# Kernel tuning notes

Hardware: AMD Instinct MI355X
Metric: run time of the kernel (lower is better)

The kernel has to match this reference:

```python
import jax, jax.numpy as jnp
import numpy as np

N = 50000   # nodes
E = 800000  # edges (avg degree 16)
D = 128     # embedding_size
K = 4096    # number of candidate result nodes (resmask.sum())


def setup_inputs() -> dict:
    key = jax.random.key(0)
    ks = jax.random.split(key, 14)
    scale = 1.0 / np.sqrt(D)
    input_node = jax.random.normal(ks[0], (N, D), jnp.float32)
    inputad = jax.random.randint(ks[1], (2, E), 0, N, dtype=jnp.int32)
    res = jax.random.uniform(ks[2], (N,), jnp.float32)
    # first-K-ones mask so masked_select has a static shape [K, D]
    resmask = jnp.concatenate([jnp.ones((K,), jnp.int32), jnp.zeros((N - K,), jnp.int32)])
    params = dict(
        W1=jax.random.normal(ks[3], (D, D), jnp.float32) * scale,
        a_src1=jax.random.normal(ks[4], (D,), jnp.float32) * scale,
        a_dst1=jax.random.normal(ks[5], (D,), jnp.float32) * scale,
        b1=jnp.zeros((D,), jnp.float32),
        W2=jax.random.normal(ks[6], (D, D), jnp.float32) * scale,
        a_src2=jax.random.normal(ks[7], (D,), jnp.float32) * scale,
        a_dst2=jax.random.normal(ks[8], (D,), jnp.float32) * scale,
        b2=jnp.zeros((D,), jnp.float32),
        w_lin=jax.random.normal(ks[9], (D,), jnp.float32) * scale,
        b_lin=jnp.zeros((), jnp.float32),
    )
    return dict(input_node=input_node, inputad=inputad, res=res,
                resmask=resmask, num_res=K, **params)


def _gat_layer(x, src, dst, W, a_src, a_dst, b):
    """PyG GATConv, heads=1, concat=False, negative_slope=0.2."""
    n = x.shape[0]
    h = x @ W                          # [N, D]
    alpha_src = h @ a_src              # [N]
    alpha_dst = h @ a_dst              # [N]
    e = jax.nn.leaky_relu(alpha_src[src] + alpha_dst[dst], 0.2)  # [E']
    # softmax over incoming edges per destination node (stable)
    emax = jax.ops.segment_max(e, dst, num_segments=n)
    ee = jnp.exp(e - emax[dst])
    denom = jax.ops.segment_sum(ee, dst, num_segments=n)
    alpha = ee / (denom[dst] + 1e-16)
    out = jax.ops.segment_sum(h[src] * alpha[:, None], dst, num_segments=n)
    return out + b


def reference(input_node, inputad, res, resmask, num_res,
              W1, a_src1, a_dst1, b1, W2, a_src2, a_dst2, b2, w_lin, b_lin):
    n = input_node.shape[0]
    # GATConv default add_self_loops=True
    loops = jnp.arange(n, dtype=inputad.dtype)
    src = jnp.concatenate([inputad[0], loops])
    dst = jnp.concatenate([inputad[1], loops])
    x = jax.nn.relu(_gat_layer(input_node, src, dst, W1, a_src1, a_dst1, b1))
    x = jax.nn.relu(_gat_layer(x, src, dst, W2, a_src2, a_dst2, b2))  # dropout = identity (eval)
    # masked_select of whole rows; resmask = first num_res ones -> static slice
    s = x[:num_res]                    # [K, D]
    li = x @ w_lin + b_lin             # [N]
    li = jnp.where(resmask == 0, -1e9, li)
    resSoftmax = jax.nn.softmax(li, axis=-1)
    loss = -(jnp.log(jnp.clip(resSoftmax, 1e-10, 1.0)) * res).sum(axis=-1)
    return (loss, resSoftmax, x, resmask, s)
```

## Files before the change

### kernel.cpp

```cpp
#include <hip/hip_runtime.h>

#define D 128
#define CACHE 8
#define BCAP 4096
#define CPAD 16
#define SCH 4096

typedef __attribute__((ext_vector_type(8))) short bf16x8;
typedef __attribute__((ext_vector_type(4))) float f32x4;

__device__ __forceinline__ unsigned fenc(float f) {
    unsigned u = __float_as_uint(f);
    return (u & 0x80000000u) ? ~u : (u | 0x80000000u);
}
__device__ __forceinline__ float fdec(unsigned u) {
    return (u & 0x80000000u) ? __uint_as_float(u ^ 0x80000000u) : __uint_as_float(~u);
}
__device__ __forceinline__ unsigned short f2b(float f) {
    unsigned u = __float_as_uint(f);
    return (unsigned short)((u + 0x7fffu + ((u >> 16) & 1u)) >> 16);
}

__global__ void zero_init(int* __restrict__ bcnt, int* __restrict__ bcur,
                          unsigned* __restrict__ limax_u, float* __restrict__ sumexp,
                          float* __restrict__ out0) {
    int t = blockIdx.x * blockDim.x + threadIdx.x;
    if (t < 512 * CPAD) {
        bcnt[t] = 0;
        bcur[t] = 0;
    }
    if (t == 0) {
        *limax_u = 0u;
        *sumexp = 0.f;
        *out0 = 0.f;
    }
}

__device__ __forceinline__ void pack_body(const float* __restrict__ W,
                                          unsigned short* __restrict__ Wp, int idx) {
    int j  = idx & 7;
    int l  = (idx >> 3) & 63;
    int ks = (idx >> 9) & 3;
    int ct = idx >> 11;
    int k = ks * 32 + ((l >> 4) << 3) + j;
    int c = ct * 16 + (l & 15);
    Wp[idx] = f2b(W[(size_t)k * D + c]);
}

__global__ void prep(const float* __restrict__ in, unsigned short* __restrict__ out,
                     const float* __restrict__ W1, unsigned short* __restrict__ Wp1,
                     const float* __restrict__ W2, unsigned short* __restrict__ Wp2,
                     const int* __restrict__ ad, int E, int n, int* __restrict__ bcnt,
                     int count8, int nbconv, int nbhist) {
    __shared__ int scnt[512];
    int b = blockIdx.x;
    int t = threadIdx.x;
    if (b < nbhist) {
        int Et = E + n;
        int base = b * SCH;
        int m = min(SCH, Et - base);
        for (int i = t; i < 512; i += 256) scnt[i] = 0;
        __syncthreads();
        for (int i = t; i < m; i += 256) {
            int e = base + i;
            int dst = (e < E) ? ad[E + e] : (e - E);
            atomicAdd(&scnt[dst >> 7], 1);
        }
        __syncthreads();
        for (int i = t; i < 512; i += 256)
            if (scnt[i]) atomicAdd(&bcnt[i * CPAD], scnt[i]);
    } else if (b < nbhist + nbconv) {
        int i = (b - nbhist) * 256 + t;
        if (i >= count8) return;
        const float4* p = (const float4*)(in + (size_t)i * 8);
        float4 a = p[0], bb = p[1];
        bf16x8 o;
        o[0] = (short)f2b(a.x);  o[1] = (short)f2b(a.y);
        o[2] = (short)f2b(a.z);  o[3] = (short)f2b(a.w);
        o[4] = (short)f2b(bb.x); o[5] = (short)f2b(bb.y);
        o[6] = (short)f2b(bb.z); o[7] = (short)f2b(bb.w);
        *(bf16x8*)(out + (size_t)i * 8) = o;
    } else if (b < nbhist + nbconv + 64) {
        pack_body(W1, Wp1, (b - nbhist - nbconv) * 256 + t);
    } else {
        pack_body(W2, Wp2, (b - nbhist - nbconv - 64) * 256 + t);
    }
}

__global__ __launch_bounds__(256) void gemm_mfma(const unsigned short* __restrict__ xb,
                                                 const unsigned short* __restrict__ Wp,
                                                 const float* __restrict__ a_src,
                                                 const float* __restrict__ a_dst,
                                                 unsigned short* __restrict__ h16,
                                                 float* __restrict__ as_, float* __restrict__ ad_,
                                                 int n) {
    __shared__ float lds[4][16][132];
    int wv = threadIdx.x >> 6;
    int lane = threadIdx.x & 63;
    int base = blockIdx.x * 64 + wv * 16;
    int arow = base + (lane & 15);
    if (arow >= n) arow = n - 1;
    const bf16x8* aptr = (const bf16x8*)(xb + (size_t)arow * D + ((lane >> 4) << 3));
    const bf16x8* bp = (const bf16x8*)Wp;

    f32x4 acc[8];
#pragma unroll
    for (int ct = 0; ct < 8; ++ct) acc[ct] = (f32x4){0.f, 0.f, 0.f, 0.f};

#pragma unroll
    for (int ks = 0; ks < 4; ++ks) {
        bf16x8 af = aptr[ks * 4];
#pragma unroll
        for (int ct = 0; ct < 8; ++ct) {
            bf16x8 bf_ = bp[(ct * 4 + ks) * 64 + lane];
            acc[ct] = __builtin_amdgcn_mfma_f32_16x16x32_bf16(af, bf_, acc[ct], 0, 0, 0);
        }
    }

    int r0 = (lane >> 4) * 4;
    int c0 = lane & 15;
#pragma unroll
    for (int ct = 0; ct < 8; ++ct)
#pragma unroll
        for (int i = 0; i < 4; ++i)
            lds[wv][r0 + i][ct * 16 + c0] = acc[ct][i];
    __syncthreads();

#pragma unroll
    for (int i = 0; i < 4; ++i) {
        int r = (lane >> 4) + i * 4;
        int gr = base + r;
        if (gr < n) {
            const float* row = lds[wv][r];
            bf16x8 o;
#pragma unroll
            for (int j = 0; j < 8; ++j) o[j] = (short)f2b(row[c0 * 8 + j]);
            *(bf16x8*)(h16 + (size_t)gr * D + c0 * 8) = o;
        }
    }

    int r = lane >> 2, q = lane & 3;
    float s1 = 0.f, s2 = 0.f;
    const float* row = lds[wv][r];
#pragma unroll
    for (int c = 0; c < 32; ++c) {
        float hv = row[q * 32 + c];
        s1 = fmaf(hv, a_src[q * 32 + c], s1);
        s2 = fmaf(hv, a_dst[q * 32 + c], s2);
    }
    s1 += __shfl_xor(s1, 1); s1 += __shfl_xor(s1, 2);
    s2 += __shfl_xor(s2, 1); s2 += __shfl_xor(s2, 2);
    int gr = base + r;
    if (q == 0 && gr < n) { as_[gr] = s1; ad_[gr] = s2; }
}


__global__ void bucket_scan(const int* __restrict__ bcnt, int* __restrict__ bbase, int nbk) {
    __shared__ int lds[512];
    int t = threadIdx.x;
    int v = (t < nbk) ? bcnt[t * CPAD] : 0;
    lds[t] = v;
    __syncthreads();
    for (int off = 1; off < 512; off <<= 1) {
        int o = (t >= off) ? lds[t - off] : 0;
        __syncthreads();
        lds[t] += o;
        __syncthreads();
    }
    if (t < nbk) bbase[t] = lds[t] - v;
}

__global__ __launch_bounds__(256) void bucket_scatter(const int* __restrict__ ad, int E, int n,
                                                      const int* __restrict__ bbase,
                                                      int* __restrict__ bcur,
                                                      unsigned* __restrict__ pairbuf) {
    __shared__ unsigned es[SCH];
    __shared__ unsigned bp[SCH];
    __shared__ int cnt[512], gofs[512];
    int t = threadIdx.x;
    int Et = E + n;
    int base = blockIdx.x * SCH;
    int m = min(SCH, Et - base);
    for (int i = t; i < 512; i += 256) cnt[i] = 0;
    __syncthreads();
    for (int i = t; i < m; i += 256) {
        int e = base + i;
        int src, dst;
        if (e < E) { src = ad[e]; dst = ad[E + e]; }
        else       { src = dst = e - E; }
        int b = dst >> 7;
        int lpos = atomicAdd(&cnt[b], 1);
        es[i] = ((unsigned)src << 7) | (unsigned)(dst & 127);
        bp[i] = ((unsigned)b << 16) | (unsigned)lpos;
    }
    __syncthreads();
    for (int i = t; i < 512; i += 256) {
        int c = cnt[i];
        gofs[i] = c ? atomicAdd(&bcur[i * CPAD], c) : 0;
    }
    __syncthreads();
    for (int i = t; i < m; i += 256) {
        unsigned v = bp[i];
        int b = v >> 16;
        int lpos = v & 0xffff;
        pairbuf[bbase[b] + gofs[b] + lpos] = es[i];
    }
}

__global__ __launch_bounds__(256) void csr_build(const unsigned* __restrict__ pairbuf,
                                                 const int* __restrict__ bbase,
                                                 int* __restrict__ deg, int* __restrict__ startv,
                                                 int* __restrict__ csr_src,
                                                 int nbk, int n, int total) {
    __shared__ unsigned es[BCAP];
    __shared__ int h[128], sc[128], cur[128];
    int b = blockIdx.x;
    int t = threadIdx.x;
    int lo = bbase[b];
    int hi = (b + 1 < nbk) ? bbase[b + 1] : total;
    int cnt = hi - lo;
    if (t < 128) h[t] = 0;
    __syncthreads();
    for (int i = t; i < cnt; i += 256) {
        unsigned p = pairbuf[lo + i];
        if (i < BCAP) es[i] = p;
        atomicAdd(&h[p & 127], 1);
    }
    __syncthreads();
    if (t < 128) sc[t] = h[t];
    __syncthreads();
    for (int off = 1; off < 128; off <<= 1) {
        int v2 = 0;
        if (t < 128 && t >= off) v2 = sc[t - off];
        __syncthreads();
        if (t < 128) sc[t] += v2;
        __syncthreads();
    }
    int dbase = b << 7;
    if (t < 128) {
        int node = dbase + t;
        if (node < n) {
            deg[node] = h[t];
            startv[node] = lo + sc[t] - h[t];
        }
        cur[t] = 0;
    }
    __syncthreads();
    for (int i = t; i < cnt; i += 256) {
        unsigned p = (i < BCAP) ? es[i] : pairbuf[lo + i];
        int dloc = p & 127;
        int pos = atomicAdd(&cur[dloc], 1);
        csr_src[lo + (sc[dloc] - h[dloc]) + pos] = (int)(p >> 7);
    }
}

__global__ void gat_aggregate(const int* __restrict__ csr_src, const int* __restrict__ start,
                              const int* __restrict__ deg, const float* __restrict__ as_,
                              const float* __restrict__ ad_, const unsigned short* __restrict__ h16,
                              const float* __restrict__ bias,
                              unsigned short* __restrict__ out16,
                              float* __restrict__ xout, float* __restrict__ sout,
                              const float* __restrict__ w_lin, const float* __restrict__ b_lin,
                              const int* __restrict__ resmask, float* __restrict__ pr,
                              const int* __restrict__ num_res, int n) {
    int wid = threadIdx.x >> 6;
    int lane = threadIdx.x & 63;
    int node = blockIdx.x * 4 + wid;
    if (node >= n) return;
    int s0 = start[node];
    int dg = deg[node];
    float adv = ad_[node];

    float acc0 = 0.f, acc1 = 0.f;

    if (dg <= 64) {
        bool ok = lane < dg;
        int sj = ok ? csr_src[s0 + lane] : 0;
        float v = -3.4e38f;
        if (ok) {
            v = as_[sj] + adv;
            v = v >= 0.f ? v : 0.2f * v;
        }
        float m = v;
        for (int off = 32; off; off >>= 1) m = fmaxf(m, __shfl_xor(m, off));
        float e = ok ? __expf(v - m) : 0.f;
        float ds = e;
        for (int off = 32; off; off >>= 1) ds += __shfl_xor(ds, off);
        float inv = 1.f / (ds + 1e-16f);

        int mc8 = (dg + 7) & ~7;
        for (int l = 0; l < mc8; l += 8) {
            float a[8];
            int   tt[8];
            unsigned hh[8];
#pragma unroll
            for (int k = 0; k < 8; ++k) {
                a[k]  = __shfl(e, l + k);
                tt[k] = __shfl(sj, l + k);
            }
#pragma unroll
            for (int k = 0; k < 8; ++k)
                hh[k] = *(const unsigned*)(h16 + (size_t)tt[k] * D + lane * 2);
#pragma unroll
            for (int k = 0; k < 8; ++k) {
                acc0 = fmaf(a[k], __uint_as_float(hh[k] << 16), acc0);
                acc1 = fmaf(a[k], __uint_as_float(hh[k] & 0xffff0000u), acc1);
            }
        }
        acc0 *= inv;
        acc1 *= inv;
    } else {
        float vreg[CACHE];
        int   sreg[CACHE];
        float m = -3.4e38f;
#pragma unroll
        for (int c = 0; c < CACHE; ++c) {
            int j = c * 64 + lane;
            bool ok = j < dg;
            int s = ok ? csr_src[s0 + j] : 0;
            sreg[c] = s;
            float v = -3.4e38f;
            if (ok) {
                v = as_[s] + adv;
                v = v >= 0.f ? v : 0.2f * v;
            }
            vreg[c] = v;
            m = fmaxf(m, v);
        }
        for (int off = 32; off; off >>= 1) m = fmaxf(m, __shfl_xor(m, off));
        float dsum = 0.f;
#pragma unroll
        for (int c = 0; c < CACHE; ++c) {
            int j = c * 64 + lane;
            float e = (j < dg) ? __expf(vreg[c] - m) : 0.f;
            vreg[c] = e;
            dsum += e;
        }
        for (int off = 32; off; off >>= 1) dsum += __shfl_xor(dsum, off);
        float inv = 1.f / (dsum + 1e-16f);
#pragma unroll
        for (int c = 0; c < CACHE; ++c) {
            if (c * 64 < dg) {
                int mc = min(64, dg - c * 64);
                for (int l = 0; l < mc; ++l) {
                    float a   = __shfl(vreg[c], l) * inv;
                    int  srcj = __shfl(sreg[c], l);
                    unsigned hv = *(const unsigned*)(h16 + (size_t)srcj * D + lane * 2);
                    acc0 = fmaf(a, __uint_as_float(hv << 16), acc0);
                    acc1 = fmaf(a, __uint_as_float(hv & 0xffff0000u), acc1);
                }
            }
        }
    }

    float2 bv = *(const float2*)(bias + lane * 2);
    float o0 = acc0 + bv.x, o1 = acc1 + bv.y;
    o0 = o0 > 0.f ? o0 : 0.f;
    o1 = o1 > 0.f ? o1 : 0.f;

    if (out16) {
        ushort2 u2;
        u2.x = f2b(o0);
        u2.y = f2b(o1);
        *(ushort2*)(out16 + (size_t)node * D + lane * 2) = u2;
    } else {
        *(float2*)(xout + (size_t)node * D + lane * 2) = make_float2(o0, o1);
        if (node < num_res[0])
            *(float2*)(sout + (size_t)node * D + lane * 2) = make_float2(o0, o1);
        float2 wv = *(const float2*)(w_lin + lane * 2);
        float part = fmaf(o0, wv.x, o1 * wv.y);
        for (int off = 32; off; off >>= 1) part += __shfl_xor(part, off);
        if (lane == 0) {
            float s = part + b_lin[0];
            if (resmask[node] == 0) s = -1000000000.0f;
            pr[node] = s;
        }
    }
}


__global__ void head_max(const float* __restrict__ pr, unsigned* __restrict__ limax_u, int n) {
    unsigned mx = 0u;
    for (int i = blockIdx.x * blockDim.x + threadIdx.x; i < n; i += gridDim.x * blockDim.x) {
        unsigned e = fenc(pr[i]);
        mx = mx > e ? mx : e;
    }
    for (int off = 32; off; off >>= 1) {
        unsigned o = __shfl_xor(mx, off);
        mx = mx > o ? mx : o;
    }
    if ((threadIdx.x & 63) == 0) atomicMax(limax_u, mx);
}

__global__ void head_exp(float* __restrict__ pr, const unsigned* __restrict__ limax_u,
                         float* __restrict__ sumexp, const int* __restrict__ resmask,
                         float* __restrict__ maskf, int n) {
    int i = blockIdx.x * blockDim.x + threadIdx.x;
    float m = fdec(*limax_u);
    float u = 0.f;
    if (i < n) {
        u = expf(pr[i] - m);
        pr[i] = u;
        maskf[i] = (float)resmask[i];
    }
    float t = u;
    for (int off = 32; off; off >>= 1) t += __shfl_down(t, off);
    if ((threadIdx.x & 63) == 0) atomicAdd(sumexp, t);
}

__global__ void head_final(float* __restrict__ pr, const float* __restrict__ sumexp,
                           const float* __restrict__ res, float* __restrict__ loss_out, int n) {
    int i = blockIdx.x * blockDim.x + threadIdx.x;
    float lt = 0.f;
    if (i < n) {
        float p = pr[i] / (*sumexp);
        pr[i] = p;
        float pc = fminf(fmaxf(p, 1e-10f), 1.0f);
        lt = -logf(pc) * res[i];
    }
    float t = lt;
    for (int off = 32; off; off >>= 1) t += __shfl_down(t, off);
    if ((threadIdx.x & 63) == 0) atomicAdd(loss_out, t);
}

extern "C" void kernel_launch(void* const* d_in, const int* in_sizes, int n_in,
                              void* d_out, int out_size, void* d_ws, size_t ws_size,
                              hipStream_t stream) {
    const float* input_node = (const float*)d_in[0];
    const int*   inputad    = (const int*)d_in[1];
    const float* res        = (const float*)d_in[2];
    const int*   resmask    = (const int*)d_in[3];
    const int*   num_res    = (const int*)d_in[4];
    const float* W1     = (const float*)d_in[5];
    const float* a_src1 = (const float*)d_in[6];
    const float* a_dst1 = (const float*)d_in[7];
    const float* b1     = (const float*)d_in[8];
    const float* W2     = (const float*)d_in[9];
    const float* a_src2 = (const float*)d_in[10];
    const float* a_dst2 = (const float*)d_in[11];
    const float* b2     = (const float*)d_in[12];
    const float* w_lin  = (const float*)d_in[13];
    const float* b_lin  = (const float*)d_in[14];

    int n = in_sizes[0] / D;
    int E = in_sizes[1] / 2;
    int Et = E + n;
    int nbk = (n + 127) >> 7;

    char* w = (char*)d_ws;
    unsigned short* xb16 = (unsigned short*)w; w += (size_t)n * D * 2;
    unsigned short* h16  = (unsigned short*)w; w += (size_t)n * D * 2;
    unsigned short* Wp1 = (unsigned short*)w; w += 16384 * 2;
    unsigned short* Wp2 = (unsigned short*)w; w += 16384 * 2;
    float* as_   = (float*)w; w += (size_t)n * 4;
    float* ad_   = (float*)w; w += (size_t)n * 4;
    int*   deg   = (int*)w;   w += (size_t)n * 4;
    int*   startv= (int*)w;   w += (size_t)n * 4;
    int*   csr_src=(int*)w;   w += (size_t)Et * 4;
    unsigned* pairbuf = (unsigned*)w; w += (size_t)Et * 4;
    int*   bbase = (int*)w;   w += 512 * 4;
    int*   bcnt  = (int*)w;   w += 512 * CPAD * 4;
    int*   bcur  = (int*)w;   w += 512 * CPAD * 4;
    unsigned* limax_u = (unsigned*)w; w += 8;
    float* sumexp = (float*)w; w += 8;

    float* out0  = (float*)d_out;
    float* prob  = out0 + 1;
    float* xout  = prob + n;
    float* maskf = xout + (size_t)n * D;
    float* sout  = maskf + n;

    dim3 blk(256);
    auto cdiv = [](long long a, long long b) { return (unsigned)((a + b - 1) / b); };
    unsigned nb = cdiv(n, 256);

    zero_init<<<32, blk, 0, stream>>>(bcnt, bcur, limax_u, sumexp, out0);

    int count8 = n * D / 8;
    unsigned nbconv = cdiv(count8, 256);
    unsigned nbhist = cdiv(Et, SCH);
    prep<<<nbhist + nbconv + 128, blk, 0, stream>>>(input_node, xb16, W1, Wp1, W2, Wp2,
                                                    inputad, E, n, bcnt, count8,
                                                    (int)nbconv, (int)nbhist);

    bucket_scan<<<1, 512, 0, stream>>>(bcnt, bbase, nbk);
    bucket_scatter<<<nbhist, blk, 0, stream>>>(inputad, E, n, bbase, bcur, pairbuf);
    csr_build<<<nbk, blk, 0, stream>>>(pairbuf, bbase, deg, startv, csr_src, nbk, n, Et);

    unsigned agg_grid = cdiv(n, 4);
    unsigned gemm_grid = cdiv(n, 64);

    gemm_mfma<<<gemm_grid, blk, 0, stream>>>(xb16, Wp1, a_src1, a_dst1, h16, as_, ad_, n);
    gat_aggregate<<<agg_grid, blk, 0, stream>>>(csr_src, startv, deg, as_, ad_, h16, b1,
                                                xb16, nullptr, nullptr, nullptr, nullptr,
                                                nullptr, nullptr, nullptr, n);

    gemm_mfma<<<gemm_grid, blk, 0, stream>>>(xb16, Wp2, a_src2, a_dst2, h16, as_, ad_, n);
    gat_aggregate<<<agg_grid, blk, 0, stream>>>(csr_src, startv, deg, as_, ad_, h16, b2,
                                                nullptr, xout, sout, w_lin, b_lin,
                                                resmask, prob, num_res, n);

    head_max<<<196, blk, 0, stream>>>(prob, limax_u, n);
    head_exp<<<nb, blk, 0, stream>>>(prob, limax_u, sumexp, resmask, maskf, n);
    head_final<<<nb, blk, 0, stream>>>(prob, sumexp, res, out0, n);
}
```

Before: 198.5 us.

## Fuse layer-1 GEMM with edge bucket scatter, widen buckets, drop scan kernel

Buckets now cover 256 destination nodes instead of 128, so there are half as many buckets. The bucket prefix scan moves into each scatter block and into csr_build, which removes the separate bucket_scan launch. The scatter blocks are merged into the same launch as the layer-1 MFMA GEMM through dynamic shared memory, so the two independent stages can overlap and one launch is saved. The aggregation loop gathers 16 neighbors per step instead of 8, and head_max uses fewer blocks. The cost is redundant scan work in every block, larger LDS use that may lower occupancy, more register pressure in the aggregation loop, and bigger per-bucket sorts with BCAP raised to 8192.

```diff
diff --git a/kernel.cpp b/kernel.cpp
--- a/kernel.cpp
+++ b/kernel.cpp
@@ -2,9 +2,13 @@
 
 #define D 128
 #define CACHE 8
-#define BCAP 4096
+#define BSH 8
+#define BCAP 8192
 #define CPAD 16
 #define SCH 4096
+
+#define GEMM_LDS 33792
+#define SCAT_LDS 35840
 
 typedef __attribute__((ext_vector_type(8))) short bf16x8;
 typedef __attribute__((ext_vector_type(4))) float f32x4;
@@ -25,7 +29,7 @@
                           unsigned* __restrict__ limax_u, float* __restrict__ sumexp,
                           float* __restrict__ out0) {
     int t = blockIdx.x * blockDim.x + threadIdx.x;
-    if (t < 512 * CPAD) {
+    if (t < 256 * CPAD) {
         bcnt[t] = 0;
         bcur[t] = 0;
     }
@@ -52,23 +56,22 @@
                      const float* __restrict__ W2, unsigned short* __restrict__ Wp2,
                      const int* __restrict__ ad, int E, int n, int* __restrict__ bcnt,
                      int count8, int nbconv, int nbhist) {
-    __shared__ int scnt[512];
+    __shared__ int scnt[256];
     int b = blockIdx.x;
     int t = threadIdx.x;
     if (b < nbhist) {
         int Et = E + n;
         int base = b * SCH;
         int m = min(SCH, Et - base);
-        for (int i = t; i < 512; i += 256) scnt[i] = 0;
+        scnt[t] = 0;
         __syncthreads();
         for (int i = t; i < m; i += 256) {
             int e = base + i;
             int dst = (e < E) ? ad[E + e] : (e - E);
-            atomicAdd(&scnt[dst >> 7], 1);
-        }
-        __syncthreads();
-        for (int i = t; i < 512; i += 256)
-            if (scnt[i]) atomicAdd(&bcnt[i * CPAD], scnt[i]);
+            atomicAdd(&scnt[dst >> BSH], 1);
+        }
+        __syncthreads();
+        if (scnt[t]) atomicAdd(&bcnt[t * CPAD], scnt[t]);
     } else if (b < nbhist + nbconv) {
         int i = (b - nbhist) * 256 + t;
         if (i >= count8) return;
@@ -87,6 +90,71 @@
     }
 }
 
+__device__ void gemm_body(char* smem, int bid, const unsigned short* __restrict__ xb,
+                          const unsigned short* __restrict__ Wp,
+                          const float* __restrict__ a_src, const float* __restrict__ a_dst,
+                          unsigned short* __restrict__ h16,
+                          float* __restrict__ as_, float* __restrict__ ad_, int n) {
+    float (*lds)[16][132] = (float (*)[16][132])smem;
+    int wv = threadIdx.x >> 6;
+    int lane = threadIdx.x & 63;
+    int base = bid * 64 + wv * 16;
+    int arow = base + (lane & 15);
+    if (arow >= n) arow = n - 1;
+    const bf16x8* aptr = (const bf16x8*)(xb + (size_t)arow * D + ((lane >> 4) << 3));
+    const bf16x8* bp = (const bf16x8*)Wp;
+
+    f32x4 acc[8];
+#pragma unroll
+    for (int ct = 0; ct < 8; ++ct) acc[ct] = (f32x4){0.f, 0.f, 0.f, 0.f};
+
+#pragma unroll
+    for (int ks = 0; ks < 4; ++ks) {
+        bf16x8 af = aptr[ks * 4];
+#pragma unroll
+        for (int ct = 0; ct < 8; ++ct) {
+            bf16x8 bf_ = bp[(ct * 4 + ks) * 64 + lane];
+            acc[ct] = __builtin_amdgcn_mfma_f32_16x16x32_bf16(af, bf_, acc[ct], 0, 0, 0);
+        }
+    }
+
+    int r0 = (lane >> 4) * 4;
+    int c0 = lane & 15;
+#pragma unroll
+    for (int ct = 0; ct < 8; ++ct)
+#pragma unroll
+        for (int i = 0; i < 4; ++i)
+            lds[wv][r0 + i][ct * 16 + c0] = acc[ct][i];
+    __syncthreads();
+
+#pragma unroll
+    for (int i = 0; i < 4; ++i) {
+        int r = (lane >> 4) + i * 4;
+        int gr = base + r;
+        if (gr < n) {
+            const float* row = lds[wv][r];
+            bf16x8 o;
+#pragma unroll
+            for (int j = 0; j < 8; ++j) o[j] = (short)f2b(row[c0 * 8 + j]);
+            *(bf16x8*)(h16 + (size_t)gr * D + c0 * 8) = o;
+        }
+    }
+
+    int r = lane >> 2, q = lane & 3;
+    float s1 = 0.f, s2 = 0.f;
+    const float* row = lds[wv][r];
+#pragma unroll
+    for (int c = 0; c < 32; ++c) {
+        float hv = row[q * 32 + c];
+        s1 = fmaf(hv, a_src[q * 32 + c], s1);
+        s2 = fmaf(hv, a_dst[q * 32 + c], s2);
+    }
+    s1 += __shfl_xor(s1, 1); s1 += __shfl_xor(s1, 2);
+    s2 += __shfl_xor(s2, 1); s2 += __shfl_xor(s2, 2);
+    int gr = base + r;
+    if (q == 0 && gr < n) { as_[gr] = s1; ad_[gr] = s2; }
+}
+
 __global__ __launch_bounds__(256) void gemm_mfma(const unsigned short* __restrict__ xb,
                                                  const unsigned short* __restrict__ Wp,
                                                  const float* __restrict__ a_src,
@@ -94,163 +162,118 @@
                                                  unsigned short* __restrict__ h16,
                                                  float* __restrict__ as_, float* __restrict__ ad_,
                                                  int n) {
-    __shared__ float lds[4][16][132];
-    int wv = threadIdx.x >> 6;
-    int lane = threadIdx.x & 63;
-    int base = blockIdx.x * 64 + wv * 16;
-    int arow = base + (lane & 15);
-    if (arow >= n) arow = n - 1;
-    const bf16x8* aptr = (const bf16x8*)(xb + (size_t)arow * D + ((lane >> 4) << 3));
-    const bf16x8* bp = (const bf16x8*)Wp;
-
-    f32x4 acc[8];
-#pragma unroll
-    for (int ct = 0; ct < 8; ++ct) acc[ct] = (f32x4){0.f, 0.f, 0.f, 0.f};
-
-#pragma unroll
-    for (int ks = 0; ks < 4; ++ks) {
-        bf16x8 af = aptr[ks * 4];
-#pragma unroll
-        for (int ct = 0; ct < 8; ++ct) {
-            bf16x8 bf_ = bp[(ct * 4 + ks) * 64 + lane];
-            acc[ct] = __builtin_amdgcn_mfma_f32_16x16x32_bf16(af, bf_, acc[ct], 0, 0, 0);
-        }
-    }
-
-    int r0 = (lane >> 4) * 4;
-    int c0 = lane & 15;
-#pragma unroll
-    for (int ct = 0; ct < 8; ++ct)
-#pragma unroll
-        for (int i = 0; i < 4; ++i)
-            lds[wv][r0 + i][ct * 16 + c0] = acc[ct][i];
-    __syncthreads();
-
-#pragma unroll
-    for (int i = 0; i < 4; ++i) {
-        int r = (lane >> 4) + i * 4;
-        int gr = base + r;
-        if (gr < n) {
-            const float* row = lds[wv][r];
-            bf16x8 o;
-#pragma unroll
-            for (int j = 0; j < 8; ++j) o[j] = (short)f2b(row[c0 * 8 + j]);
-            *(bf16x8*)(h16 + (size_t)gr * D + c0 * 8) = o;
-        }
-    }
-
-    int r = lane >> 2, q = lane & 3;
-    float s1 = 0.f, s2 = 0.f;
-    const float* row = lds[wv][r];
-#pragma unroll
-    for (int c = 0; c < 32; ++c) {
-        float hv = row[q * 32 + c];
-        s1 = fmaf(hv, a_src[q * 32 + c], s1);
-        s2 = fmaf(hv, a_dst[q * 32 + c], s2);
-    }
-    s1 += __shfl_xor(s1, 1); s1 += __shfl_xor(s1, 2);
-    s2 += __shfl_xor(s2, 1); s2 += __shfl_xor(s2, 2);
-    int gr = base + r;
-    if (q == 0 && gr < n) { as_[gr] = s1; ad_[gr] = s2; }
-}
-
-
-__global__ void bucket_scan(const int* __restrict__ bcnt, int* __restrict__ bbase, int nbk) {
-    __shared__ int lds[512];
+    extern __shared__ char smem[];
+    gemm_body(smem, blockIdx.x, xb, Wp, a_src, a_dst, h16, as_, ad_, n);
+}
+
+__device__ void scatter_body(char* smem, int sb, const int* __restrict__ ad, int E, int n,
+                             const int* __restrict__ bcnt, int* __restrict__ bcur,
+                             unsigned* __restrict__ pairbuf, int nbk) {
+    unsigned* es = (unsigned*)smem;
+    unsigned* bp = es + SCH;
+    int* cnt  = (int*)(bp + SCH);
+    int* gofs = cnt + 256;
+    int* bs   = gofs + 256;
     int t = threadIdx.x;
     int v = (t < nbk) ? bcnt[t * CPAD] : 0;
-    lds[t] = v;
-    __syncthreads();
-    for (int off = 1; off < 512; off <<= 1) {
-        int o = (t >= off) ? lds[t - off] : 0;
-        __syncthreads();
-        lds[t] += o;
-        __syncthreads();
-    }
-    if (t < nbk) bbase[t] = lds[t] - v;
-}
-
-__global__ __launch_bounds__(256) void bucket_scatter(const int* __restrict__ ad, int E, int n,
-                                                      const int* __restrict__ bbase,
-                                                      int* __restrict__ bcur,
-                                                      unsigned* __restrict__ pairbuf) {
-    __shared__ unsigned es[SCH];
-    __shared__ unsigned bp[SCH];
-    __shared__ int cnt[512], gofs[512];
-    int t = threadIdx.x;
+    bs[t] = v;
+    __syncthreads();
+    for (int off = 1; off < 256; off <<= 1) {
+        int o = (t >= off) ? bs[t - off] : 0;
+        __syncthreads();
+        bs[t] += o;
+        __syncthreads();
+    }
+    int incl = bs[t];
+    __syncthreads();
+    bs[t] = incl - v;
+    cnt[t] = 0;
+    __syncthreads();
+
     int Et = E + n;
-    int base = blockIdx.x * SCH;
+    int base = sb * SCH;
     int m = min(SCH, Et - base);
-    for (int i = t; i < 512; i += 256) cnt[i] = 0;
-    __syncthreads();
     for (int i = t; i < m; i += 256) {
         int e = base + i;
         int src, dst;
         if (e < E) { src = ad[e]; dst = ad[E + e]; }
         else       { src = dst = e - E; }
-        int b = dst >> 7;
+        int b = dst >> BSH;
         int lpos = atomicAdd(&cnt[b], 1);
-        es[i] = ((unsigned)src << 7) | (unsigned)(dst & 127);
+        es[i] = ((unsigned)src << BSH) | (unsigned)(dst & 255);
         bp[i] = ((unsigned)b << 16) | (unsigned)lpos;
     }
     __syncthreads();
-    for (int i = t; i < 512; i += 256) {
-        int c = cnt[i];
-        gofs[i] = c ? atomicAdd(&bcur[i * CPAD], c) : 0;
-    }
+    gofs[t] = cnt[t] ? atomicAdd(&bcur[t * CPAD], cnt[t]) : 0;
     __syncthreads();
     for (int i = t; i < m; i += 256) {
-        unsigned v = bp[i];
-        int b = v >> 16;
-        int lpos = v & 0xffff;
-        pairbuf[bbase[b] + gofs[b] + lpos] = es[i];
-    }
+        unsigned vv = bp[i];
+        int b = vv >> 16;
+        int lpos = vv & 0xffff;
+        pairbuf[bs[b] + gofs[b] + lpos] = es[i];
+    }
+}
+
+__global__ __launch_bounds__(256) void gemm1_scatter(
+        const unsigned short* __restrict__ xb, const unsigned short* __restrict__ Wp,
+        const float* __restrict__ a_src, const float* __restrict__ a_dst,
+        unsigned short* __restrict__ h16, float* __restrict__ as_, float* __restrict__ ad_,
+        const int* __restrict__ ad, int E, const int* __restrict__ bcnt, int* __restrict__ bcur,
+        unsigned* __restrict__ pairbuf, int nbk, int n, int ggrid) {
+    extern __shared__ char smem[];
+    if ((int)blockIdx.x < ggrid)
+        gemm_body(smem, blockIdx.x, xb, Wp, a_src, a_dst, h16, as_, ad_, n);
+    else
+        scatter_body(smem, blockIdx.x - ggrid, ad, E, n, bcnt, bcur, pairbuf, nbk);
 }
 
 __global__ __launch_bounds__(256) void csr_build(const unsigned* __restrict__ pairbuf,
-                                                 const int* __restrict__ bbase,
+                                                 const int* __restrict__ bcnt,
                                                  int* __restrict__ deg, int* __restrict__ startv,
-                                                 int* __restrict__ csr_src,
-                                                 int nbk, int n, int total) {
+                                                 int* __restrict__ csr_src, int nbk, int n) {
     __shared__ unsigned es[BCAP];
-    __shared__ int h[128], sc[128], cur[128];
+    __shared__ int bs[256], h[256], sc[256], cur[256];
     int b = blockIdx.x;
     int t = threadIdx.x;
-    int lo = bbase[b];
-    int hi = (b + 1 < nbk) ? bbase[b + 1] : total;
-    int cnt = hi - lo;
-    if (t < 128) h[t] = 0;
+    int v = (t < nbk) ? bcnt[t * CPAD] : 0;
+    bs[t] = v;
+    __syncthreads();
+    for (int off = 1; off < 256; off <<= 1) {
+        int o = (t >= off) ? bs[t - off] : 0;
+        __syncthreads();
+        bs[t] += o;
+        __syncthreads();
+    }
+    int lo = bs[b] - bcnt[b * CPAD];
+    int cnt = bcnt[b * CPAD];
+    h[t] = 0;
     __syncthreads();
     for (int i = t; i < cnt; i += 256) {
         unsigned p = pairbuf[lo + i];
         if (i < BCAP) es[i] = p;
-        atomicAdd(&h[p & 127], 1);
-    }
-    __syncthreads();
-    if (t < 128) sc[t] = h[t];
-    __syncthreads();
-    for (int off = 1; off < 128; off <<= 1) {
-        int v2 = 0;
-        if (t < 128 && t >= off) v2 = sc[t - off];
-        __syncthreads();
-        if (t < 128) sc[t] += v2;
-        __syncthreads();
-    }
-    int dbase = b << 7;
-    if (t < 128) {
-        int node = dbase + t;
-        if (node < n) {
-            deg[node] = h[t];
-            startv[node] = lo + sc[t] - h[t];
-        }
-        cur[t] = 0;
-    }
+        atomicAdd(&h[p & 255], 1);
+    }
+    __syncthreads();
+    sc[t] = h[t];
+    __syncthreads();
+    for (int off = 1; off < 256; off <<= 1) {
+        int v2 = (t >= off) ? sc[t - off] : 0;
+        __syncthreads();
+        sc[t] += v2;
+        __syncthreads();
+    }
+    int node = (b << BSH) + t;
+    if (node < n) {
+        deg[node] = h[t];
+        startv[node] = lo + sc[t] - h[t];
+    }
+    cur[t] = 0;
     __syncthreads();
     for (int i = t; i < cnt; i += 256) {
         unsigned p = (i < BCAP) ? es[i] : pairbuf[lo + i];
-        int dloc = p & 127;
+        int dloc = p & 255;
         int pos = atomicAdd(&cur[dloc], 1);
-        csr_src[lo + (sc[dloc] - h[dloc]) + pos] = (int)(p >> 7);
+        csr_src[lo + (sc[dloc] - h[dloc]) + pos] = (int)(p >> BSH);
     }
 }
 
@@ -288,21 +311,21 @@
         for (int off = 32; off; off >>= 1) ds += __shfl_xor(ds, off);
         float inv = 1.f / (ds + 1e-16f);
 
-        int mc8 = (dg + 7) & ~7;
-        for (int l = 0; l < mc8; l += 8) {
-            float a[8];
-            int   tt[8];
-            unsigned hh[8];
-#pragma unroll
-            for (int k = 0; k < 8; ++k) {
+        int mc16 = (dg + 15) & ~15;
+        for (int l = 0; l < mc16; l += 16) {
+            float a[16];
+            int   tt[16];
+            unsigned hh[16];
+#pragma unroll
+            for (int k = 0; k < 16; ++k) {
                 a[k]  = __shfl(e, l + k);
                 tt[k] = __shfl(sj, l + k);
             }
 #pragma unroll
-            for (int k = 0; k < 8; ++k)
+            for (int k = 0; k < 16; ++k)
                 hh[k] = *(const unsigned*)(h16 + (size_t)tt[k] * D + lane * 2);
 #pragma unroll
-            for (int k = 0; k < 8; ++k) {
+            for (int k = 0; k < 16; ++k) {
                 acc0 = fmaf(a[k], __uint_as_float(hh[k] << 16), acc0);
                 acc1 = fmaf(a[k], __uint_as_float(hh[k] & 0xffff0000u), acc1);
             }
@@ -445,7 +468,7 @@
     int n = in_sizes[0] / D;
     int E = in_sizes[1] / 2;
     int Et = E + n;
-    int nbk = (n + 127) >> 7;
+    int nbk = (n + 255) >> BSH;
 
     char* w = (char*)d_ws;
     unsigned short* xb16 = (unsigned short*)w; w += (size_t)n * D * 2;
@@ -458,9 +481,8 @@
     int*   startv= (int*)w;   w += (size_t)n * 4;
     int*   csr_src=(int*)w;   w += (size_t)Et * 4;
     unsigned* pairbuf = (unsigned*)w; w += (size_t)Et * 4;
-    int*   bbase = (int*)w;   w += 512 * 4;
-    int*   bcnt  = (int*)w;   w += 512 * CPAD * 4;
-    int*   bcur  = (int*)w;   w += 512 * CPAD * 4;
+    int*   bcnt  = (int*)w;   w += 256 * CPAD * 4;
+    int*   bcur  = (int*)w;   w += 256 * CPAD * 4;
     unsigned* limax_u = (unsigned*)w; w += 8;
     float* sumexp = (float*)w; w += 8;
 
@@ -483,24 +505,25 @@
                                                     inputad, E, n, bcnt, count8,
                                                     (int)nbconv, (int)nbhist);
 
-    bucket_scan<<<1, 512, 0, stream>>>(bcnt, bbase, nbk);
-    bucket_scatter<<<nbhist, blk, 0, stream>>>(inputad, E, n, bbase, bcur, pairbuf);
-    csr_build<<<nbk, blk, 0, stream>>>(pairbuf, bbase, deg, startv, csr_src, nbk, n, Et);
-
     unsigned agg_grid = cdiv(n, 4);
     unsigned gemm_grid = cdiv(n, 64);
 
-    gemm_mfma<<<gemm_grid, blk, 0, stream>>>(xb16, Wp1, a_src1, a_dst1, h16, as_, ad_, n);
+    gemm1_scatter<<<gemm_grid + nbhist, blk, SCAT_LDS, stream>>>(
+        xb16, Wp1, a_src1, a_dst1, h16, as_, ad_,
+        inputad, E, bcnt, bcur, pairbuf, nbk, n, (int)gemm_grid);
+
+    csr_build<<<nbk, blk, 0, stream>>>(pairbuf, bcnt, deg, startv, csr_src, nbk, n);
+
     gat_aggregate<<<agg_grid, blk, 0, stream>>>(csr_src, startv, deg, as_, ad_, h16, b1,
                                                 xb16, nullptr, nullptr, nullptr, nullptr,
                                                 nullptr, nullptr, nullptr, n);
 
-    gemm_mfma<<<gemm_grid, blk, 0, stream>>>(xb16, Wp2, a_src2, a_dst2, h16, as_, ad_, n);
+    gemm_mfma<<<gemm_grid, blk, GEMM_LDS, stream>>>(xb16, Wp2, a_src2, a_dst2, h16, as_, ad_, n);
     gat_aggregate<<<agg_grid, blk, 0, stream>>>(csr_src, startv, deg, as_, ad_, h16, b2,
                                                 nullptr, xout, sout, w_lin, b_lin,
                                                 resmask, prob, num_res, n);
 
-    head_max<<<196, blk, 0, stream>>>(prob, limax_u, n);
+    head_max<<<64, blk, 0, stream>>>(prob, limax_u, n);
     head_exp<<<nb, blk, 0, stream>>>(prob, limax_u, sumexp, resmask, maskf, n);
     head_final<<<nb, blk, 0, stream>>>(prob, sumexp, res, out0, n);
 }
```

Measured after the change: 195.2 us. Within noise of the previous version (-1.7%).
